# Optimization experiments

Hardware: AMD Instinct MI355X
Metric: run time of the kernel (lower is better)

The kernel has to match this reference:

```python
import jax, jax.numpy as jnp
import numpy as np
from jax import lax


def conv2d(x, w, b=None, stride=1, pad=0):
    y = lax.conv_general_dilated(x, w, (stride, stride), [(pad, pad), (pad, pad)],
                                 dimension_numbers=('NCHW', 'OIHW', 'NCHW'))
    if b is not None:
        y = y + b[None, :, None, None]
    return y


def bilinear_resize_ac(S, Ho, Wo):
    # F.interpolate(..., mode='bilinear', align_corners=True)
    B, C, H, W = S.shape
    ys = jnp.linspace(0.0, H - 1.0, Ho)
    xs = jnp.linspace(0.0, W - 1.0, Wo)
    y0 = jnp.floor(ys).astype(jnp.int32); y1 = jnp.minimum(y0 + 1, H - 1); wy = ys - y0
    x0 = jnp.floor(xs).astype(jnp.int32); x1 = jnp.minimum(x0 + 1, W - 1); wx = xs - x0
    Sy = S[:, :, y0, :] * (1 - wy)[None, None, :, None] + S[:, :, y1, :] * wy[None, None, :, None]
    return Sy[:, :, :, x0] * (1 - wx)[None, None, None, :] + Sy[:, :, :, x1] * wx[None, None, None, :]


def deform_conv(x, offset, weight, bias=None, mask=None, stride=1, pad=1, dil=1):
    # (Modulated) deformable conv, deformable_groups=1; DCNv2 semantics:
    # offset channels are (dy, dx) pairs per kernel tap; zero padding outside.
    B, C, H, W = x.shape
    O, Ci, kh, kw = weight.shape
    K = kh * kw
    Ho, Wo = offset.shape[2], offset.shape[3]
    off = offset.reshape(B, K, 2, Ho, Wo)
    kyy, kxx = jnp.meshgrid(jnp.arange(kh) * dil, jnp.arange(kw) * dil, indexing='ij')
    kyy = kyy.reshape(K).astype(x.dtype); kxx = kxx.reshape(K).astype(x.dtype)
    base_y = (jnp.arange(Ho) * stride - pad).astype(x.dtype)
    base_x = (jnp.arange(Wo) * stride - pad).astype(x.dtype)
    py = base_y[None, None, :, None] + kyy[None, :, None, None] + off[:, :, 0]  # [B,K,Ho,Wo]
    px = base_x[None, None, None, :] + kxx[None, :, None, None] + off[:, :, 1]
    y0 = jnp.floor(py); x0 = jnp.floor(px)
    dy = py - y0; dx = px - x0
    y0i = y0.astype(jnp.int32); x0i = x0.astype(jnp.int32)
    xf = x.reshape(B, C, H * W)

    def corner(yi, xi, w):
        valid = (yi >= 0) & (yi <= H - 1) & (xi >= 0) & (xi <= W - 1)
        yc = jnp.clip(yi, 0, H - 1); xc = jnp.clip(xi, 0, W - 1)
        idx = (yc * W + xc).reshape(B, -1)  # [B, K*Ho*Wo]
        g = jax.vmap(lambda f, i: f[:, i])(xf, idx)  # [B, C, K*Ho*Wo]
        g = g.reshape(B, C, K, Ho, Wo)
        return g * (w * valid.astype(x.dtype))[:, None]

    s = (corner(y0i, x0i, (1 - dy) * (1 - dx))
         + corner(y0i, x0i + 1, (1 - dy) * dx)
         + corner(y0i + 1, x0i, dy * (1 - dx))
         + corner(y0i + 1, x0i + 1, dy * dx))  # [B,C,K,Ho,Wo]
    if mask is not None:
        s = s * mask[:, None]  # [B,1,K,Ho,Wo]
    out = jnp.einsum('bckhw,ock->bohw', s, weight.reshape(O, Ci, K))
    if bias is not None:
        out = out + bias[None, :, None, None]
    return out


def setup_inputs():
    key = jax.random.key(0)
    ks = jax.random.split(key, 16)
    B, Cin, Cout, H, W = 8, 256, 256, 64, 64

    def n(k, shape, s):
        return jax.random.normal(k, shape, jnp.float32) * s

    return {
        'x': jax.random.normal(ks[0], (B, Cin, H, W), jnp.float32),
        'S': jax.random.normal(ks[1], (B, 3, 128, 128), jnp.float32),
        'sp_w1': n(ks[2], (64, 3, 3, 3), 0.2), 'sp_b1': jnp.zeros(64), 'sp_s1': jnp.ones(64) + n(ks[3], (64,), 0.05), 'sp_o1': n(ks[3], (64,), 0.05),
        'sp_w2': n(ks[4], (64, 64, 3, 3), 0.05), 'sp_b2': jnp.zeros(64), 'sp_s2': jnp.ones(64) + n(ks[5], (64,), 0.05), 'sp_o2': n(ks[5], (64,), 0.05),
        'sp_w3': n(ks[6], (64, 64, 3, 3), 0.05), 'sp_b3': jnp.zeros(64), 'sp_s3': jnp.ones(64) + n(ks[7], (64,), 0.05), 'sp_o3': n(ks[7], (64,), 0.05),
        'off_w': n(ks[8], (18, 64, 3, 3), 0.05), 'off_b': jnp.zeros(18),
        'dc_off_w': n(ks[9], (18, 64, 3, 3), 0.05), 'dc_off_b': jnp.zeros(18),
        'dc_w': n(ks[10], (64, 64, 3, 3), 0.04),
        'm_w': n(ks[11], (9, 64, 1, 1), 0.1), 'm_b': jnp.zeros(9),
        'weight': n(ks[12], (Cout, Cin, 3, 3), 0.02), 'bias': jnp.zeros(Cout),
    }


def reference(x, S, sp_w1, sp_b1, sp_s1, sp_o1, sp_w2, sp_b2, sp_s2, sp_o2,
              sp_w3, sp_b3, sp_s3, sp_o3, off_w, off_b, dc_off_w, dc_off_b,
              dc_w, m_w, m_b, weight, bias):
    H, W = x.shape[2], x.shape[3]
    Si = bilinear_resize_ac(S, H, W)
    h = jax.nn.relu(conv2d(Si, sp_w1, sp_b1, 1, 1) * sp_s1[None, :, None, None] + sp_o1[None, :, None, None])
    h = jax.nn.relu(conv2d(h, sp_w2, sp_b2, 1, 1) * sp_s2[None, :, None, None] + sp_o2[None, :, None, None])
    h = jax.nn.relu(conv2d(h, sp_w3, sp_b3, 1, 1) * sp_s3[None, :, None, None] + sp_o3[None, :, None, None])
    offset = conv2d(h, off_w, off_b, 1, 1)                 # [B,18,H,W]
    dc_off = conv2d(h, dc_off_w, dc_off_b, 1, 1)           # internal offsets of weight_generator1 (DCNv1)
    feat = deform_conv(h, dc_off, dc_w, None, None, 1, 1, 1)
    mask = jax.nn.sigmoid(conv2d(feat, m_w, m_b, 1, 0))    # [B,9,H,W]
    return deform_conv(x, offset, weight, bias, mask, 1, 1, 1)
```

## Files before the change

kernel.cpp:

```cpp
#include <hip/hip_runtime.h>
#include <hip/hip_bf16.h>

typedef unsigned short u16;
typedef unsigned int u32;
typedef __attribute__((ext_vector_type(8))) short short8;
typedef __attribute__((ext_vector_type(4))) unsigned short ush4;
typedef __attribute__((ext_vector_type(16))) float f32x16;

#define OXT   0
#define OSI   (OXT + 8388608)
#define OA    (OSI + 98304)
#define OB    (OA + 2097152)
#define OC    (OB + 2097152)
#define OOFFS (OC + 2097152)
#define OMSK  (OOFFS + 1179648)
#define OWT   (OMSK + 294912)
#define OWSP1 (OWT + 589824)
#define OBSP1 (OWSP1 + 1728)
#define OWSP2 (OBSP1 + 64)
#define OBSP2 (OWSP2 + 36864)
#define OWSP3 (OBSP2 + 64)
#define OBSP3 (OWSP3 + 36864)
#define OWOFF (OBSP3 + 64)
#define OBOFF (OWOFF + 36864)
#define OWDC  (OBOFF + 64)

__device__ __forceinline__ u16 f2bf(float f) {
    __hip_bfloat16 hb = __float2bfloat16(f);
    return __builtin_bit_cast(u16, hb);
}
__device__ __forceinline__ float bf2f(u16 v) {
    return __builtin_bit_cast(float, (u32)v << 16);
}
__device__ __forceinline__ int sswz(int kg, int px) {
    return (px & ~7) | ((px ^ kg) & 7);
}

__device__ __forceinline__ void corner_tab_big(
    int tap, int pix0, int b, int gp,
    const float* __restrict__ offs, const float* __restrict__ maskb,
    int* car, float* cwr)
{
    int pix = pix0 + gp; int pib = pix & 4095;
    int y = pib >> 6, x = pib & 63;
    float offy = offs[(size_t)pix * 36 + tap * 2];
    float offx = offs[(size_t)pix * 36 + tap * 2 + 1];
    float m = maskb[(size_t)pix * 9 + tap];
    float py = (float)(y - 1 + tap / 3) + offy;
    float pxf = (float)(x - 1 + (tap % 3)) + offx;
    float fy = floorf(py), fx = floorf(pxf);
    int y0 = (int)fy, x0 = (int)fx;
    float dyf = py - fy, dxf = pxf - fx;
    #pragma unroll
    for (int j = 0; j < 4; j++) {
        float wj = ((j >> 1) ? dyf : 1.f - dyf) * ((j & 1) ? dxf : 1.f - dxf);
        int yy = y0 + (j >> 1), xx = x0 + (j & 1);
        bool valid = (yy >= 0 && yy < 64 && xx >= 0 && xx < 64);
        int yc = min(max(yy, 0), 63), xc = min(max(xx, 0), 63);
        car[j] = (b * 4096 + yc * 64 + xc) << 8;
        cwr[j] = valid ? wj * m : 0.f;
    }
}

__device__ __forceinline__ void corner_tab_small(
    int tap, int pix0, int b, int gp,
    const float* __restrict__ offs, int* car, float* cwr)
{
    int pix = pix0 + gp; int pib = pix & 4095;
    int y = pib >> 6, x = pib & 63;
    float offy = offs[(size_t)pix * 36 + 18 + tap * 2];
    float offx = offs[(size_t)pix * 36 + 18 + tap * 2 + 1];
    float py = (float)(y - 1 + tap / 3) + offy;
    float pxf = (float)(x - 1 + (tap % 3)) + offx;
    float fy = floorf(py), fx = floorf(pxf);
    int y0 = (int)fy, x0 = (int)fx;
    float dyf = py - fy, dxf = pxf - fx;
    #pragma unroll
    for (int j = 0; j < 4; j++) {
        float wj = ((j >> 1) ? dyf : 1.f - dyf) * ((j & 1) ? dxf : 1.f - dxf);
        int yy = y0 + (j >> 1), xx = x0 + (j & 1);
        bool valid = (yy >= 0 && yy < 64 && xx >= 0 && xx < 64);
        int yc = min(max(yy, 0), 63), xc = min(max(xx, 0), 63);
        car[j] = (b * 4096 + yc * 64 + xc) << 6;
        cwr[j] = valid ? wj : 0.f;
    }
}

__global__ __launch_bounds__(256) void prologue_k(
    const float* __restrict__ weight,
    const float* __restrict__ sp_w1, const float* __restrict__ sp_s1,
    const float* __restrict__ sp_w2, const float* __restrict__ sp_s2,
    const float* __restrict__ sp_w3, const float* __restrict__ sp_s3,
    const float* __restrict__ off_w, const float* __restrict__ dc_off_w,
    const float* __restrict__ dc_w,
    const float* __restrict__ sp_b1, const float* __restrict__ sp_o1,
    const float* __restrict__ sp_b2, const float* __restrict__ sp_o2,
    const float* __restrict__ sp_b3, const float* __restrict__ sp_o3,
    const float* __restrict__ off_b, const float* __restrict__ dc_off_b,
    const float* __restrict__ x, const float* __restrict__ S,
    float* __restrict__ ws)
{
    __shared__ float tile[64][65];
    int blk = blockIdx.x;
    int t = threadIdx.x;

    if (blk >= 4936) {
        int i = (blk - 4936) * 256 + t;
        if (i >= 8 * 64 * 64 * 3) return;
        int c = i % 3; int xq = (i / 3) & 63; int y = (i / 192) & 63; int b = i / 12288;
        const float sc = 127.0f / 63.0f;
        float sy = y * sc, sx = xq * sc;
        float fy = floorf(sy), fx = floorf(sx);
        int y0 = (int)fy, x0 = (int)fx;
        int y1 = min(y0 + 1, 127), x1 = min(x0 + 1, 127);
        float wy = sy - fy, wx = sx - fx;
        const float* Sb = S + (size_t)(b * 3 + c) * 16384;
        float v00 = Sb[y0 * 128 + x0], v01 = Sb[y0 * 128 + x1];
        float v10 = Sb[y1 * 128 + x0], v11 = Sb[y1 * 128 + x1];
        (ws + OSI)[i] = (v00 * (1.f - wy) + v10 * wy) * (1.f - wx)
                      + (v01 * (1.f - wy) + v11 * wy) * wx;
        return;
    }
    if (blk >= 2888) {
        int bb = blk - 2888;
        int chunk = bb & 3; int by = bb >> 2;
        int b = by >> 6; int y = by & 63;
        int c0 = chunk * 64;
        u16* xT = (u16*)(ws + OXT);
        for (int i = t; i < 4096; i += 256) {
            int ci = i >> 6, xi = i & 63;
            tile[ci][xi] = x[((b * 256 + c0 + ci) * 64 + y) * 64 + xi];
        }
        __syncthreads();
        for (int i = t; i < 4096; i += 256) {
            int xi = i >> 6, ci = i & 63;
            xT[((b * 64 + y) * 64 + xi) * 256 + c0 + ci] = f2bf(tile[ci][xi]);
        }
        return;
    }
    int i = blk * 256 + t;
    if (i < 589824) {
        int j = i & 7; int o = (i >> 3) & 255; int kg = i >> 11;
        int K = kg * 8 + j; int k = K >> 8; int c = K & 255;
        ((u16*)(ws + OWT))[i] = f2bf(weight[o * 2304 + c * 9 + k]);
        return;
    }
    i -= 589824;
    if (i < 1728) {
        int o = i & 63; int kc = i >> 6; int c = kc % 3; int k = kc / 3;
        ws[OWSP1 + i] = sp_w1[(o * 3 + c) * 9 + k] * sp_s1[o];
        return;
    }
    i -= 1728;
    if (i < 36864) {
        int e = i & 7; int o = (i >> 3) & 63; int kg = (i >> 9) & 7; int tp = i >> 12;
        ((u16*)(ws + OWSP2))[i] = f2bf(sp_w2[(o * 64 + kg * 8 + e) * 9 + tp] * sp_s2[o]);
        return;
    }
    i -= 36864;
    if (i < 36864) {
        int e = i & 7; int o = (i >> 3) & 63; int kg = (i >> 9) & 7; int tp = i >> 12;
        ((u16*)(ws + OWSP3))[i] = f2bf(sp_w3[(o * 64 + kg * 8 + e) * 9 + tp] * sp_s3[o]);
        return;
    }
    i -= 36864;
    if (i < 36864) {
        int e = i & 7; int o = (i >> 3) & 63; int kg = (i >> 9) & 7; int tp = i >> 12;
        int c = kg * 8 + e;
        float v = 0.f;
        if (o < 18) v = off_w[(o * 64 + c) * 9 + tp];
        else if (o < 36) v = dc_off_w[((o - 18) * 64 + c) * 9 + tp];
        ((u16*)(ws + OWOFF))[i] = f2bf(v);
        return;
    }
    i -= 36864;
    if (i < 36864) {
        int e = i & 7; int o = (i >> 3) & 63; int kg = (i >> 9) & 7; int tp = i >> 12;
        ((u16*)(ws + OWDC))[i] = f2bf(dc_w[(o * 64 + kg * 8 + e) * 9 + tp]);
        return;
    }
    i -= 36864;
    if (i < 64) { ws[OBSP1 + i] = sp_b1[i] * sp_s1[i] + sp_o1[i]; return; }
    i -= 64;
    if (i < 64) { ws[OBSP2 + i] = sp_b2[i] * sp_s2[i] + sp_o2[i]; return; }
    i -= 64;
    if (i < 64) { ws[OBSP3 + i] = sp_b3[i] * sp_s3[i] + sp_o3[i]; return; }
    i -= 64;
    if (i < 64) { ws[OBOFF + i] = (i < 18) ? off_b[i] : (i < 36 ? dc_off_b[i - 18] : 0.f); return; }
}

__global__ __launch_bounds__(256) void conv_in_k(const float* __restrict__ in,
                                                 const float* __restrict__ wt,
                                                 const float* __restrict__ bias,
                                                 u16* __restrict__ out)
{
    __shared__ float rows[3][66][3];
    int by = blockIdx.x; int b = by >> 6; int y = by & 63;
    int t = threadIdx.x;
    for (int i = t; i < 3 * 66 * 3; i += 256) {
        int r = i / 198; int rem = i - r * 198;
        int xi = rem / 3; int c = rem - xi * 3;
        int yy = y - 1 + r, xx = xi - 1;
        float v = 0.f;
        if (yy >= 0 && yy < 64 && xx >= 0 && xx < 64)
            v = in[(((b * 64 + yy) * 64 + xx) * 3) + c];
        rows[r][xi][c] = v;
    }
    __syncthreads();
    int o4 = (t & 15) * 4; int xg = t >> 4;
    float acc[4][4];
    #pragma unroll
    for (int oi = 0; oi < 4; oi++) {
        float bv = bias[o4 + oi];
        #pragma unroll
        for (int xi = 0; xi < 4; xi++) acc[oi][xi] = bv;
    }
    for (int k = 0; k < 9; k++) {
        int dy = k / 3, dx = k - 3 * (k / 3);
        for (int c = 0; c < 3; c++) {
            float4 w = *reinterpret_cast<const float4*>(&wt[(k * 3 + c) * 64 + o4]);
            #pragma unroll
            for (int xi = 0; xi < 4; xi++) {
                float iv = rows[dy][xg * 4 + xi + dx][c];
                acc[0][xi] = fmaf(w.x, iv, acc[0][xi]);
                acc[1][xi] = fmaf(w.y, iv, acc[1][xi]);
                acc[2][xi] = fmaf(w.z, iv, acc[2][xi]);
                acc[3][xi] = fmaf(w.w, iv, acc[3][xi]);
            }
        }
    }
    #pragma unroll
    for (int xi = 0; xi < 4; xi++) {
        int x = xg * 4 + xi;
        ush4 v;
        v.x = f2bf(fmaxf(acc[0][xi], 0.f));
        v.y = f2bf(fmaxf(acc[1][xi], 0.f));
        v.z = f2bf(fmaxf(acc[2][xi], 0.f));
        v.w = f2bf(fmaxf(acc[3][xi], 0.f));
        *reinterpret_cast<ush4*>(&out[((size_t)(by * 64 + x)) * 64 + o4]) = v;
    }
}

template <int MODE, bool RELU>
__global__ __launch_bounds__(512) void conv_mfma_k(const u16* __restrict__ in,
                                                   const u16* __restrict__ wm,
                                                   const float* __restrict__ bias,
                                                   u16* __restrict__ outH,
                                                   float* __restrict__ outF)
{
    __shared__ __attribute__((aligned(16))) char lds_h[4 * 66 * 128];
    __shared__ __attribute__((aligned(16))) u16 wtap[9][8][64][8];

    int t = threadIdx.x;
    int b = blockIdx.x >> 5; int y0 = (blockIdx.x & 31) * 2;
    int pix0 = b * 4096 + y0 * 64;
    int wid = t >> 6, lane = t & 63;
    int lrow = lane & 31, lhi = lane >> 5;
    int o0 = (wid & 1) << 5;
    int px0 = (wid >> 1) << 5;
    int px = px0 + lrow;
    int ry_l = px >> 6, xc = px & 63;

    for (int i = t; i < 4 * 66 * 8; i += 512) {
        int r = i / 528; int rem = i - r * 528;
        int xi = rem >> 3; int g = rem & 7;
        int yy = y0 - 1 + r, xx = xi - 1;
        short8 v = {0,0,0,0,0,0,0,0};
        if (yy >= 0 && yy < 64 && xx >= 0 && xx < 64)
            v = *reinterpret_cast<const short8*>(&in[(size_t)((b * 4096 + yy * 64 + xx)) * 64 + g * 8]);
        int byte = (r * 66 + xi) * 128 + ((g * 16) ^ ((xi & 7) << 4));
        *reinterpret_cast<short8*>(lds_h + byte) = v;
    }
    {
        const char* gb = (const char*)wm;
        char* lb = (char*)&wtap[0][0][0][0];
        #pragma unroll
        for (int i = 0; i < 9; i++) {
            int off = i * 8192 + wid * 1024;
            __builtin_amdgcn_global_load_lds(
                (const __attribute__((address_space(1))) void*)(gb + off + lane * 16),
                (__attribute__((address_space(3))) void*)(lb + off), 16, 0, 0);
        }
    }
    __syncthreads();

    f32x16 acc;
    #pragma unroll
    for (int r = 0; r < 16; r++) acc[r] = 0.f;

    #pragma unroll
    for (int tap = 0; tap < 9; tap++) {
        int dy = tap / 3, dx = tap - 3 * (tap / 3);
        int xi = xc + dx;
        int rowbyte = ((ry_l + dy) * 66 + xi) * 128;
        int swz = (xi & 7) << 4;
        #pragma unroll
        for (int ks = 0; ks < 4; ks++) {
            int kg = ks * 2 + lhi;
            short8 a0 = *reinterpret_cast<const short8*>(&wtap[tap][kg][o0 + lrow][0]);
            short8 b0 = *reinterpret_cast<const short8*>(lds_h + rowbyte + ((kg * 16) ^ swz));
            acc = __builtin_amdgcn_mfma_f32_32x32x16_bf16(a0, b0, acc, 0, 0, 0);
        }
    }
    __syncthreads();

    if (MODE == 0) {
        #pragma unroll
        for (int q = 0; q < 4; q++) {
            int ob = o0 + q * 8 + 4 * lhi;
            #pragma unroll
            for (int h = 0; h < 2; h++) {
                float v0 = acc[q * 4 + h * 2] + bias[ob + h * 2];
                float v1 = acc[q * 4 + h * 2 + 1] + bias[ob + h * 2 + 1];
                if (RELU) { v0 = fmaxf(v0, 0.f); v1 = fmaxf(v1, 0.f); }
                u32 pk = (u32)f2bf(v0) | ((u32)f2bf(v1) << 16);
                int byte = px * 128 + (((ob + h * 2) * 2) ^ ((px & 7) << 4));
                *reinterpret_cast<u32*>(lds_h + byte) = pk;
            }
        }
        __syncthreads();
        #pragma unroll
        for (int i = 0; i < 2; i++) {
            int cid = i * 512 + t;
            int p = cid >> 3, g = cid & 7;
            short8 v = *reinterpret_cast<const short8*>(lds_h + p * 128 + ((g * 16) ^ ((p & 7) << 4)));
            *reinterpret_cast<short8*>(&outH[(size_t)(pix0 + p) * 64 + g * 8]) = v;
        }
    } else {
        float* ltf = (float*)lds_h;
        #pragma unroll
        for (int r = 0; r < 16; r++) {
            int o = o0 + (r & 3) + ((r >> 2) << 3) + (lhi << 2);
            if (o < 36) ltf[px * 40 + o] = acc[r] + bias[o];
        }
        __syncthreads();
        for (int i = t; i < 1152; i += 512) {
            int p = i / 9, q = i - 9 * (i / 9);
            float4 v = *reinterpret_cast<const float4*>(&ltf[p * 40 + q * 4]);
            *reinterpret_cast<float4*>(&outF[(size_t)(pix0 + p) * 36 + q * 4]) = v;
        }
    }
}

__global__ __launch_bounds__(512) void dconv_small_mfma(
    const u16* __restrict__ h, const float* __restrict__ offs,
    const u16* __restrict__ wdc, const float* __restrict__ m_w,
    const float* __restrict__ m_b, float* __restrict__ maskb)
{
    __shared__ __attribute__((aligned(16))) char smem[106496];
    u16 (*wtile)[8][64][8]  = (u16 (*)[8][64][8])smem;
    u16 (*stile)[8][128][8] = (u16 (*)[8][128][8])(smem + 73728);

    int t = threadIdx.x;
    int id = blockIdx.x;
    int blk = (id & 7) * 32 + (id >> 3);
    int pix0 = blk * 128;
    int b = pix0 >> 12;
    int wid = t >> 6, lane = t & 63;
    int lrow = lane & 31, lhi = lane >> 5;
    int o0 = (wid & 1) << 5;
    int px0 = (wid >> 1) << 5;
    int gp = t >> 2, gsub = t & 3;

    int car[4]; float cwr[4];
    short8 g[8];

    corner_tab_small(0, pix0, b, gp, offs, car, cwr);
    {
        int c = gsub << 4;
        #pragma unroll
        for (int j = 0; j < 4; j++) {
            const u16* p = h + car[j] + c;
            g[j * 2]     = *reinterpret_cast<const short8*>(p);
            g[j * 2 + 1] = *reinterpret_cast<const short8*>(p + 8);
        }
    }
    {
        const char* gb = (const char*)wdc;
        char* lb = (char*)smem;
        #pragma unroll
        for (int i = 0; i < 9; i++) {
            int off = i * 8192 + wid * 1024;
            __builtin_amdgcn_global_load_lds(
                (const __attribute__((address_space(1))) void*)(gb + off + lane * 16),
                (__attribute__((address_space(3))) void*)(lb + off), 16, 0, 0);
        }
    }
    asm volatile("s_waitcnt vmcnt(0)" ::: "memory");

    f32x16 acc;
    #pragma unroll
    for (int r = 0; r < 16; r++) acc[r] = 0.f;

    for (int tap = 0; tap < 9; ++tap) {
        int cur = tap & 1;

        float va[16];
        #pragma unroll
        for (int e = 0; e < 16; e++) va[e] = 0.f;
        #pragma unroll
        for (int j = 0; j < 4; j++) {
            float w = cwr[j];
            #pragma unroll
            for (int e = 0; e < 8; e++) {
                va[e]     = fmaf(w, bf2f((u16)g[j * 2][e]), va[e]);
                va[8 + e] = fmaf(w, bf2f((u16)g[j * 2 + 1][e]), va[8 + e]);
            }
        }
        short8 s0, s1;
        #pragma unroll
        for (int e = 0; e < 8; e++) { s0[e] = (short)f2bf(va[e]); s1[e] = (short)f2bf(va[8 + e]); }
        int kg0 = gsub * 2, kg1 = gsub * 2 + 1;
        *reinterpret_cast<short8*>(&stile[cur][kg0][sswz(kg0, gp)][0]) = s0;
        *reinterpret_cast<short8*>(&stile[cur][kg1][sswz(kg1, gp)][0]) = s1;

        if (tap < 8) {
            corner_tab_small(tap + 1, pix0, b, gp, offs, car, cwr);
            int c = gsub << 4;
            #pragma unroll
            for (int j = 0; j < 4; j++) {
                const u16* p = h + car[j] + c;
                g[j * 2]     = *reinterpret_cast<const short8*>(p);
                g[j * 2 + 1] = *reinterpret_cast<const short8*>(p + 8);
            }
        }
        asm volatile("s_waitcnt lgkmcnt(0)" ::: "memory");
        __builtin_amdgcn_s_barrier();

        #pragma unroll
        for (int ks = 0; ks < 4; ks++) {
            int kg = ks * 2 + lhi;
            short8 a0 = *reinterpret_cast<const short8*>(&wtile[tap][kg][o0 + lrow][0]);
            short8 b0 = *reinterpret_cast<const short8*>(&stile[cur][kg][sswz(kg, px0 + lrow)][0]);
            acc = __builtin_amdgcn_mfma_f32_32x32x16_bf16(a0, b0, acc, 0, 0, 0);
        }
    }

    __syncthreads();
    float* featl = (float*)smem;
    int pxl = px0 + lrow;
    #pragma unroll
    for (int r = 0; r < 16; r++) {
        int o = o0 + (r & 3) + ((r >> 2) << 3) + (lhi << 2);
        featl[pxl * 65 + o] = acc[r];
    }
    __syncthreads();
    if (t < 256) {
        int p = t >> 1, hh = t & 1;
        int pix = pix0 + p;
        const float* fr = &featl[p * 65];
        int j0 = hh ? 4 : 0, j1 = hh ? 9 : 4;
        for (int j = j0; j < j1; j++) {
            float a = m_b[j];
            #pragma unroll 8
            for (int cc = 0; cc < 64; cc++) a = fmaf(fr[cc], m_w[j * 64 + cc], a);
            maskb[(size_t)pix * 9 + j] = 1.f / (1.f + expf(-a));
        }
    }
}

__global__ __launch_bounds__(512) void dconv_big_mfma(
    const u16* __restrict__ xT, const float* __restrict__ offs,
    const float* __restrict__ maskb, const u16* __restrict__ wKg,
    const float* __restrict__ bias, float* __restrict__ out)
{
    __shared__ __attribute__((aligned(16))) u16 wtile[2][8][256][8];
    __shared__ __attribute__((aligned(16))) u16 stile[2][8][128][8];

    int t = threadIdx.x;
    int id = blockIdx.x;
    int blk = (id & 7) * 32 + (id >> 3);
    int pix0 = blk * 128;
    int b = pix0 >> 12, pib0 = pix0 & 4095;
    int wid = t >> 6, lane = t & 63;
    int lrow = lane & 31, lhi = lane >> 5;
    int o0 = (wid & 3) << 6;
    int px0 = (wid >> 2) << 6;
    int gp = t >> 2, gsub = t & 3;

    int car[4]; float cwr[4];
    short8 g[8];

    corner_tab_big(0, pix0, b, gp, offs, maskb, car, cwr);
    {
        int c = gsub << 4;
        #pragma unroll
        for (int j = 0; j < 4; j++) {
            const u16* p = xT + car[j] + c;
            g[j * 2]     = *reinterpret_cast<const short8*>(p);
            g[j * 2 + 1] = *reinterpret_cast<const short8*>(p + 8);
        }
    }
    {
        const char* gb = (const char*)wKg;
        char* lb = (char*)&wtile[0][0][0][0];
        #pragma unroll
        for (int i = 0; i < 4; i++) {
            int off = i * 8192 + wid * 1024;
            __builtin_amdgcn_global_load_lds(
                (const __attribute__((address_space(1))) void*)(gb + off + lane * 16),
                (__attribute__((address_space(3))) void*)(lb + off), 16, 0, 0);
        }
    }

    f32x16 acc[2][2];
    #pragma unroll
    for (int ao = 0; ao < 2; ao++)
        #pragma unroll
        for (int bp = 0; bp < 2; bp++)
            #pragma unroll
            for (int r = 0; r < 16; r++) acc[ao][bp][r] = 0.f;

    for (int kt = 0; kt < 36; ++kt) {
        int cur = kt & 1, nxt = cur ^ 1;

        float va[16];
        #pragma unroll
        for (int e = 0; e < 16; e++) va[e] = 0.f;
        #pragma unroll
        for (int j = 0; j < 4; j++) {
            float w = cwr[j];
            #pragma unroll
            for (int e = 0; e < 8; e++) {
                va[e]     = fmaf(w, bf2f((u16)g[j * 2][e]), va[e]);
                va[8 + e] = fmaf(w, bf2f((u16)g[j * 2 + 1][e]), va[8 + e]);
            }
        }
        short8 s0, s1;
        #pragma unroll
        for (int e = 0; e < 8; e++) { s0[e] = (short)f2bf(va[e]); s1[e] = (short)f2bf(va[8 + e]); }
        int kg0 = gsub * 2, kg1 = gsub * 2 + 1;
        *reinterpret_cast<short8*>(&stile[cur][kg0][sswz(kg0, gp)][0]) = s0;
        *reinterpret_cast<short8*>(&stile[cur][kg1][sswz(kg1, gp)][0]) = s1;

        if (kt < 35) {
            if (((kt + 1) & 3) == 0)
                corner_tab_big((kt + 1) >> 2, pix0, b, gp, offs, maskb, car, cwr);
            int c = (((kt + 1) & 3) << 6) + (gsub << 4);
            #pragma unroll
            for (int j = 0; j < 4; j++) {
                const u16* p = xT + car[j] + c;
                g[j * 2]     = *reinterpret_cast<const short8*>(p);
                g[j * 2 + 1] = *reinterpret_cast<const short8*>(p + 8);
            }
            asm volatile("s_waitcnt vmcnt(8) lgkmcnt(0)" ::: "memory");
        } else {
            asm volatile("s_waitcnt vmcnt(0) lgkmcnt(0)" ::: "memory");
        }
        __builtin_amdgcn_s_barrier();

        #pragma unroll
        for (int ks = 0; ks < 4; ks++) {
            int kg = ks * 2 + lhi;
            short8 a0 = *reinterpret_cast<const short8*>(&wtile[cur][kg][o0 + lrow][0]);
            short8 a1 = *reinterpret_cast<const short8*>(&wtile[cur][kg][o0 + 32 + lrow][0]);
            short8 b0 = *reinterpret_cast<const short8*>(&stile[cur][kg][sswz(kg, px0 + lrow)][0]);
            short8 b1 = *reinterpret_cast<const short8*>(&stile[cur][kg][sswz(kg, px0 + 32 + lrow)][0]);
            acc[0][0] = __builtin_amdgcn_mfma_f32_32x32x16_bf16(a0, b0, acc[0][0], 0, 0, 0);
            acc[0][1] = __builtin_amdgcn_mfma_f32_32x32x16_bf16(a0, b1, acc[0][1], 0, 0, 0);
            acc[1][0] = __builtin_amdgcn_mfma_f32_32x32x16_bf16(a1, b0, acc[1][0], 0, 0, 0);
            acc[1][1] = __builtin_amdgcn_mfma_f32_32x32x16_bf16(a1, b1, acc[1][1], 0, 0, 0);
        }
        if (kt < 35) {
            const char* gb = (const char*)(wKg + (size_t)(kt + 1) * 16384);
            char* lb = (char*)&wtile[nxt][0][0][0];
            #pragma unroll
            for (int i = 0; i < 4; i++) {
                int off = i * 8192 + wid * 1024;
                __builtin_amdgcn_global_load_lds(
                    (const __attribute__((address_space(1))) void*)(gb + off + lane * 16),
                    (__attribute__((address_space(3))) void*)(lb + off), 16, 0, 0);
            }
        }
    }

    #pragma unroll
    for (int ao = 0; ao < 2; ao++) {
        #pragma unroll
        for (int r = 0; r < 16; r++) {
            int o = o0 + ao * 32 + (r & 3) + ((r >> 2) << 3) + (lhi << 2);
            float bv = bias[o];
            size_t rowoff = ((size_t)(b * 256 + o) << 12) + pib0 + px0;
            out[rowoff + lrow] = acc[ao][0][r] + bv;
            out[rowoff + 32 + lrow] = acc[ao][1][r] + bv;
        }
    }
}

extern "C" void kernel_launch(void* const* d_in, const int* in_sizes, int n_in,
                              void* d_out, int out_size, void* d_ws, size_t ws_size,
                              hipStream_t stream)
{
    const float* x        = (const float*)d_in[0];
    const float* S        = (const float*)d_in[1];
    const float* sp_w1    = (const float*)d_in[2];
    const float* sp_b1    = (const float*)d_in[3];
    const float* sp_s1    = (const float*)d_in[4];
    const float* sp_o1    = (const float*)d_in[5];
    const float* sp_w2    = (const float*)d_in[6];
    const float* sp_b2    = (const float*)d_in[7];
    const float* sp_s2    = (const float*)d_in[8];
    const float* sp_o2    = (const float*)d_in[9];
    const float* sp_w3    = (const float*)d_in[10];
    const float* sp_b3    = (const float*)d_in[11];
    const float* sp_s3    = (const float*)d_in[12];
    const float* sp_o3    = (const float*)d_in[13];
    const float* off_w    = (const float*)d_in[14];
    const float* off_b    = (const float*)d_in[15];
    const float* dc_off_w = (const float*)d_in[16];
    const float* dc_off_b = (const float*)d_in[17];
    const float* dc_w     = (const float*)d_in[18];
    const float* m_w      = (const float*)d_in[19];
    const float* m_b      = (const float*)d_in[20];
    const float* weight   = (const float*)d_in[21];
    const float* bias     = (const float*)d_in[22];
    float* out = (float*)d_out;
    float* ws  = (float*)d_ws;

    u16*   xTb   = (u16*)(ws + OXT);
    float* Si    = ws + OSI;
    u16*   h1    = (u16*)(ws + OA);
    u16*   h2    = (u16*)(ws + OB);
    u16*   h3    = (u16*)(ws + OC);
    float* offsb = ws + OOFFS;
    float* maskb = ws + OMSK;

    prologue_k<<<5320, 256, 0, stream>>>(weight, sp_w1, sp_s1, sp_w2, sp_s2,
                                         sp_w3, sp_s3, off_w, dc_off_w, dc_w,
                                         sp_b1, sp_o1, sp_b2, sp_o2, sp_b3, sp_o3,
                                         off_b, dc_off_b, x, S, ws);
    conv_in_k<<<512, 256, 0, stream>>>(Si, ws + OWSP1, ws + OBSP1, h1);
    conv_mfma_k<0, true><<<256, 512, 0, stream>>>(h1, (const u16*)(ws + OWSP2),
                                                  ws + OBSP2, h2, nullptr);
    conv_mfma_k<0, true><<<256, 512, 0, stream>>>(h2, (const u16*)(ws + OWSP3),
                                                  ws + OBSP3, h3, nullptr);
    conv_mfma_k<1, false><<<256, 512, 0, stream>>>(h3, (const u16*)(ws + OWOFF),
                                                   ws + OBOFF, nullptr, offsb);
    dconv_small_mfma<<<256, 512, 0, stream>>>(h3, offsb, (const u16*)(ws + OWDC),
                                              m_w, m_b, maskb);
    dconv_big_mfma<<<256, 512, 0, stream>>>(xTb, offsb, maskb,
                                            (const u16*)(ws + OWT), bias, out);
}
```

Before: 122.5 us.

## Deepen deformable gather prefetch to two stages with double-buffered registers

The bilinear-corner gather loads of x are now issued two K-steps ahead instead of one. The gathered values and corner weights are kept in two register buffers indexed by the step parity. The goal is to hide more global-gather latency behind the MFMA work. In exchange it roughly doubles the gather register footprint and recomputes the corner table more often. It also indexes register arrays with a runtime parity, which could lower occupancy or spill to scratch.

```diff
diff --git a/kernel.cpp b/kernel.cpp
--- a/kernel.cpp
+++ b/kernel.cpp
@@ -478,17 +478,26 @@
     int px0 = (wid >> 2) << 6;
     int gp = t >> 2, gsub = t & 3;
 
-    int car[4]; float cwr[4];
-    short8 g[8];
-
-    corner_tab_big(0, pix0, b, gp, offs, maskb, car, cwr);
+    int car[4]; float cwr[2][4];
+    short8 g[2][8];
+
+    corner_tab_big(0, pix0, b, gp, offs, maskb, car, cwr[0]);
+    #pragma unroll
+    for (int j = 0; j < 4; j++) cwr[1][j] = cwr[0][j];
     {
         int c = gsub << 4;
         #pragma unroll
         for (int j = 0; j < 4; j++) {
             const u16* p = xT + car[j] + c;
-            g[j * 2]     = *reinterpret_cast<const short8*>(p);
-            g[j * 2 + 1] = *reinterpret_cast<const short8*>(p + 8);
+            g[0][j * 2]     = *reinterpret_cast<const short8*>(p);
+            g[0][j * 2 + 1] = *reinterpret_cast<const short8*>(p + 8);
+        }
+        c = 64 + (gsub << 4);
+        #pragma unroll
+        for (int j = 0; j < 4; j++) {
+            const u16* p = xT + car[j] + c;
+            g[1][j * 2]     = *reinterpret_cast<const short8*>(p);
+            g[1][j * 2 + 1] = *reinterpret_cast<const short8*>(p + 8);
         }
     }
     {
@@ -519,11 +528,11 @@
         for (int e = 0; e < 16; e++) va[e] = 0.f;
         #pragma unroll
         for (int j = 0; j < 4; j++) {
-            float w = cwr[j];
+            float w = cwr[cur][j];
             #pragma unroll
             for (int e = 0; e < 8; e++) {
-                va[e]     = fmaf(w, bf2f((u16)g[j * 2][e]), va[e]);
-                va[8 + e] = fmaf(w, bf2f((u16)g[j * 2 + 1][e]), va[8 + e]);
+                va[e]     = fmaf(w, bf2f((u16)g[cur][j * 2][e]), va[e]);
+                va[8 + e] = fmaf(w, bf2f((u16)g[cur][j * 2 + 1][e]), va[8 + e]);
             }
         }
         short8 s0, s1;
@@ -533,15 +542,15 @@
         *reinterpret_cast<short8*>(&stile[cur][kg0][sswz(kg0, gp)][0]) = s0;
         *reinterpret_cast<short8*>(&stile[cur][kg1][sswz(kg1, gp)][0]) = s1;
 
-        if (kt < 35) {
-            if (((kt + 1) & 3) == 0)
-                corner_tab_big((kt + 1) >> 2, pix0, b, gp, offs, maskb, car, cwr);
-            int c = (((kt + 1) & 3) << 6) + (gsub << 4);
+        if (kt < 34) {
+            if (((kt + 2) & 3) < 2)
+                corner_tab_big((kt + 2) >> 2, pix0, b, gp, offs, maskb, car, cwr[cur]);
+            int c = (((kt + 2) & 3) << 6) + (gsub << 4);
             #pragma unroll
             for (int j = 0; j < 4; j++) {
                 const u16* p = xT + car[j] + c;
-                g[j * 2]     = *reinterpret_cast<const short8*>(p);
-                g[j * 2 + 1] = *reinterpret_cast<const short8*>(p + 8);
+                g[cur][j * 2]     = *reinterpret_cast<const short8*>(p);
+                g[cur][j * 2 + 1] = *reinterpret_cast<const short8*>(p + 8);
             }
             asm volatile("s_waitcnt vmcnt(8) lgkmcnt(0)" ::: "memory");
         } else {
```

Result: slower. 280.7 us (+129.1%).
